# Optimization experiments

Measured on AMD Instinct MI355X. Metric: run time of the kernel, lower is better.

Reference implementation:

```python
import jax, jax.numpy as jnp
import numpy as np

IN_DIM = 18 * 2 * 1 * 536  # 19296
H = 512
OUT = 11
STEPS = 1024


def setup_inputs() -> dict:
    key = jax.random.key(0)
    ks = jax.random.split(key, 14)
    s = 0.02  # small init scale for stable LSTM dynamics
    f32 = jnp.float32
    return {
        "inputs": jax.random.normal(ks[0], (STEPS, IN_DIM), dtype=f32),
        "W_in": jax.random.normal(ks[1], (H, IN_DIM), dtype=f32) * s,
        "b_in": jnp.zeros((H,), dtype=f32),
        "Wih0": jax.random.normal(ks[2], (4 * H, H), dtype=f32) * s,
        "Whh0": jax.random.normal(ks[3], (4 * H, H), dtype=f32) * s,
        "bih0": jnp.zeros((4 * H,), dtype=f32),
        "bhh0": jnp.zeros((4 * H,), dtype=f32),
        "Wih1": jax.random.normal(ks[4], (4 * H, H), dtype=f32) * s,
        "Whh1": jax.random.normal(ks[5], (4 * H, H), dtype=f32) * s,
        "bih1": jnp.zeros((4 * H,), dtype=f32),
        "bhh1": jnp.zeros((4 * H,), dtype=f32),
        "W_out": jax.random.normal(ks[6], (OUT, H), dtype=f32) * s,
        "b_out": jnp.zeros((OUT,), dtype=f32),
    }


def _lstm_cell(gates, c):
    # PyTorch gate order: input, forget, cell(g), output
    i, f, g, o = jnp.split(gates, 4, axis=-1)
    c_new = jax.nn.sigmoid(f) * c + jax.nn.sigmoid(i) * jnp.tanh(g)
    h_new = jax.nn.sigmoid(o) * jnp.tanh(c_new)
    return h_new, c_new


def reference(inputs, W_in, b_in, Wih0, Whh0, bih0, bhh0,
              Wih1, Whh1, bih1, bhh1, W_out, b_out):
    # Input projection is time-independent -> batch it across all steps.
    x_proj = inputs @ W_in.T + b_in            # (STEPS, H)
    gx0 = x_proj @ Wih0.T + bih0               # (STEPS, 4H) precomputed layer-0 input gates

    def step(carry, gx0_t):
        h0, c0, h1, c1 = carry
        h0, c0 = _lstm_cell(gx0_t + h0 @ Whh0.T + bhh0, c0)
        h1, c1 = _lstm_cell(h0 @ Wih1.T + bih1 + h1 @ Whh1.T + bhh1, c1)
        return (h0, c0, h1, c1), h1

    z = jnp.zeros((H,), dtype=inputs.dtype)
    (h0, c0, h1, c1), hs = jax.lax.scan(step, (z, z, z, z), gx0)
    outputs = (hs @ W_out.T + b_out)[:, None, :]   # (STEPS, 1, OUT) == torch (steps, batch=1, 11)
    hn = jnp.stack([h0, h1])[:, None, :]           # (num_layers=2, batch=1, H)
    cn = jnp.stack([c0, c1])[:, None, :]
    return outputs, hn, cn
```

## Files before the change

### kernel.cpp

```cpp
#include <hip/hip_runtime.h>
#include <math.h>

typedef unsigned long long ull;
typedef unsigned int u32;
typedef unsigned short u16;
typedef _Float16 half2v __attribute__((ext_vector_type(2)));
typedef __bf16 bf16x8 __attribute__((ext_vector_type(8)));
typedef float f32x4 __attribute__((ext_vector_type(4)));

#define H 512
#define STEPS 1024
#define OUTN 11

__device__ __forceinline__ float sigm(float x) { return 1.f / (1.f + __expf(-x)); }
__device__ __forceinline__ ull ld_pair(const ull* p) {
  return __hip_atomic_load((ull*)p, __ATOMIC_RELAXED, __HIP_MEMORY_SCOPE_AGENT);
}
__device__ __forceinline__ void st_pair(ull* p, ull v) {
  __hip_atomic_store(p, v, __ATOMIC_RELAXED, __HIP_MEMORY_SCOPE_AGENT);
}
__device__ __forceinline__ float dot2acc(half2v a, half2v b, float c) {
#if __has_builtin(__builtin_amdgcn_fdot2)
  return __builtin_amdgcn_fdot2(a, b, c, false);
#else
  return c + (float)a.x * (float)b.x + (float)a.y * (float)b.y;
#endif
}
__device__ __forceinline__ u16 f16bits(float x) {
  return __builtin_bit_cast(u16, (_Float16)x);
}
__device__ __forceinline__ half2v bch2(u32 u) { return __builtin_bit_cast(half2v, u); }

__device__ __forceinline__ u32 split_bf16(float x) {
  u32 u = __float_as_uint(x);
  u32 rh = (u + 0x7FFFu + ((u >> 16) & 1u)) & 0xFFFF0000u;
  float hf = __uint_as_float(rh);
  float lo = x - hf;
  u32 ul = __float_as_uint(lo);
  u32 rl = (ul + 0x7FFFu + ((ul >> 16) & 1u)) & 0xFFFF0000u;
  return (rh >> 16) | rl;
}

__global__ void cvt_split(float* __restrict__ A, float* __restrict__ B, int nA, int n4) {
  int idx = blockIdx.x * 256 + threadIdx.x;
  if (idx >= n4) return;
  int base = idx * 4;
  float* p = (base < nA) ? (A + base) : (B + (base - nA));
  float4 v = *(float4*)p;
  u32 r0 = split_bf16(v.x), r1 = split_bf16(v.y), r2 = split_bf16(v.z), r3 = split_bf16(v.w);
  uint4 o = make_uint4(r0, r1, r2, r3);
  *(uint4*)p = o;
}

__global__ __launch_bounds__(256, 2)
void gemm_hilo(const u32* __restrict__ A2, const u32* __restrict__ B2,
               float* __restrict__ C, int M, int N, int K)
{
  __shared__ __align__(16) u16 Ah[64 * 32], Al[64 * 32], Bh[64 * 32], Bl[64 * 32];
  const int z = blockIdx.z;
  const int zstart = z * 151;
  const int nsteps = (z < 3) ? 151 : 150;
  const int mt = blockIdx.x * 64, nt = blockIdx.y * 64;
  const int tid = threadIdx.x;
  const int row = tid >> 2, cg = (tid & 3) * 8;
  const int wave = tid >> 6, lane = tid & 63;
  const int wm = (wave & 1) * 32, wn = (wave >> 1) * 32;
  const int quad = lane >> 4, l16 = lane & 15;

  f32x4 acc[2][2];
#pragma unroll
  for (int i = 0; i < 2; ++i)
#pragma unroll
    for (int j = 0; j < 2; ++j) acc[i][j] = (f32x4)0.f;

  for (int s = 0; s < nsteps; ++s) {
    const int kb = (zstart + s) * 32;
    {
      const u32* ap = A2 + (size_t)(mt + row) * K + kb + cg;
      const u32* bp = B2 + (size_t)(nt + row) * K + kb + cg;
      uint4 a0 = *(const uint4*)ap, a1 = *(const uint4*)(ap + 4);
      uint4 b0 = *(const uint4*)bp, b1 = *(const uint4*)(bp + 4);
      uint4 hi, lo;
      hi = make_uint4((a0.x & 0xFFFF) | (a0.y << 16), (a0.z & 0xFFFF) | (a0.w << 16),
                      (a1.x & 0xFFFF) | (a1.y << 16), (a1.z & 0xFFFF) | (a1.w << 16));
      lo = make_uint4((a0.x >> 16) | (a0.y & 0xFFFF0000u), (a0.z >> 16) | (a0.w & 0xFFFF0000u),
                      (a1.x >> 16) | (a1.y & 0xFFFF0000u), (a1.z >> 16) | (a1.w & 0xFFFF0000u));
      *(uint4*)&Ah[row * 32 + cg] = hi;
      *(uint4*)&Al[row * 32 + cg] = lo;
      hi = make_uint4((b0.x & 0xFFFF) | (b0.y << 16), (b0.z & 0xFFFF) | (b0.w << 16),
                      (b1.x & 0xFFFF) | (b1.y << 16), (b1.z & 0xFFFF) | (b1.w << 16));
      lo = make_uint4((b0.x >> 16) | (b0.y & 0xFFFF0000u), (b0.z >> 16) | (b0.w & 0xFFFF0000u),
                      (b1.x >> 16) | (b1.y & 0xFFFF0000u), (b1.z >> 16) | (b1.w & 0xFFFF0000u));
      *(uint4*)&Bh[row * 32 + cg] = hi;
      *(uint4*)&Bl[row * 32 + cg] = lo;
    }
    __syncthreads();
    bf16x8 ah[2], al[2], bh[2], bl[2];
#pragma unroll
    for (int mf = 0; mf < 2; ++mf) {
      int r = (wm + mf * 16 + l16) * 32 + quad * 8;
      ah[mf] = *reinterpret_cast<const bf16x8*>(&Ah[r]);
      al[mf] = *reinterpret_cast<const bf16x8*>(&Al[r]);
    }
#pragma unroll
    for (int nf = 0; nf < 2; ++nf) {
      int r = (wn + nf * 16 + l16) * 32 + quad * 8;
      bh[nf] = *reinterpret_cast<const bf16x8*>(&Bh[r]);
      bl[nf] = *reinterpret_cast<const bf16x8*>(&Bl[r]);
    }
#pragma unroll
    for (int mf = 0; mf < 2; ++mf)
#pragma unroll
      for (int nf = 0; nf < 2; ++nf) {
        acc[mf][nf] = __builtin_amdgcn_mfma_f32_16x16x32_bf16(ah[mf], bh[nf], acc[mf][nf], 0, 0, 0);
        acc[mf][nf] = __builtin_amdgcn_mfma_f32_16x16x32_bf16(ah[mf], bl[nf], acc[mf][nf], 0, 0, 0);
        acc[mf][nf] = __builtin_amdgcn_mfma_f32_16x16x32_bf16(al[mf], bh[nf], acc[mf][nf], 0, 0, 0);
      }
    __syncthreads();
  }

#pragma unroll
  for (int mf = 0; mf < 2; ++mf)
#pragma unroll
    for (int nf = 0; nf < 2; ++nf)
#pragma unroll
      for (int r = 0; r < 4; ++r) {
        int rw = mt + wm + mf * 16 + quad * 4 + r;
        int cl = nt + wn + nf * 16 + l16;
        atomicAdd(&C[(size_t)rw * N + cl], acc[mf][nf][r]);
      }
}

#define GBM 64
#define GBN 64
#define GBK 64
#define GLD 76

__global__ __launch_bounds__(256, 2)
void gemm_nt(const float* __restrict__ A, const float* __restrict__ B,
             float* __restrict__ C, const float* __restrict__ bias,
             int M, int N, int K)
{
  __shared__ float As[GBM][GLD];
  __shared__ float Bs[GBN][GLD];
  const int mt = blockIdx.x, nt = blockIdx.y;
  const int tid = threadIdx.x;
  const int tx = tid & 15, ty = tid >> 4;

  float acc[4][4] = {{0.f}};

  for (int kb = 0; kb < K; kb += GBK) {
#pragma unroll
    for (int i = 0; i < 4; ++i) {
      int r = ty + i * 16;
      int gk = kb + tx * 4;
      *(float4*)&As[r][tx * 4] = *(const float4*)(A + (size_t)(mt * GBM + r) * K + gk);
      *(float4*)&Bs[r][tx * 4] = *(const float4*)(B + (size_t)(nt * GBN + r) * K + gk);
    }
    __syncthreads();
#pragma unroll
    for (int k4 = 0; k4 < GBK; k4 += 4) {
      float4 a[4], b[4];
#pragma unroll
      for (int i = 0; i < 4; ++i) a[i] = *(const float4*)&As[ty * 4 + i][k4];
#pragma unroll
      for (int j = 0; j < 4; ++j) b[j] = *(const float4*)&Bs[tx * 4 + j][k4];
#pragma unroll
      for (int i = 0; i < 4; ++i)
#pragma unroll
        for (int j = 0; j < 4; ++j) {
          acc[i][j] = fmaf(a[i].x, b[j].x, acc[i][j]);
          acc[i][j] = fmaf(a[i].y, b[j].y, acc[i][j]);
          acc[i][j] = fmaf(a[i].z, b[j].z, acc[i][j]);
          acc[i][j] = fmaf(a[i].w, b[j].w, acc[i][j]);
        }
    }
    __syncthreads();
  }

#pragma unroll
  for (int i = 0; i < 4; ++i) {
    int m = mt * GBM + ty * 4 + i;
#pragma unroll
    for (int j = 0; j < 4; ++j) {
      int n = nt * GBN + tx * 4 + j;
      C[(size_t)m * N + n] = acc[i][j] + bias[n];
    }
  }
}

__global__ void init_xproj(float* __restrict__ xp, const float* __restrict__ b_in) {
  int i = blockIdx.x * 256 + threadIdx.x;
  xp[i] = b_in[i & (H - 1)];
}

__global__ void out_proj(const float* __restrict__ hs1, const float* __restrict__ Wout,
                         const float* __restrict__ bout, float* __restrict__ out) {
  int idx = blockIdx.x * 256 + threadIdx.x;
  if (idx >= STEPS * OUTN) return;
  int t = idx / OUTN, o = idx - t * OUTN;
  const float* h = hs1 + t * H;
  const float* wr = Wout + o * H;
  float acc = 0.f;
#pragma unroll 4
  for (int i = 0; i < H; i += 4) {
    float4 hv = *(const float4*)(h + i);
    float4 wv = *(const float4*)(wr + i);
    acc = fmaf(hv.x, wv.x, acc);
    acc = fmaf(hv.y, wv.y, acc);
    acc = fmaf(hv.z, wv.z, acc);
    acc = fmaf(hv.w, wv.w, acc);
  }
  out[idx] = acc + bout[o];
}

#define NC0 24
#define NC1 16
#define RD 8

__global__ __launch_bounds__(512, 1)
void lstm_chains(const float* __restrict__ gx0,
                 const float* __restrict__ Whh0, const float* __restrict__ bhh0,
                 const float* __restrict__ Wih1, const float* __restrict__ Whh1,
                 const float* __restrict__ bih1, const float* __restrict__ bhh1,
                 float* __restrict__ hs1, float* __restrict__ out,
                 ull* __restrict__ mb0, ull* __restrict__ mb1,
                 int* __restrict__ flags1)
{
  const int wg = blockIdx.x;
  const int tid = threadIdx.x;
  const bool role0 = (wg < 8);

  __shared__ __align__(16) u32 hl_u[512];
  __shared__ __align__(16) float gbuf[256];
  __shared__ __align__(16) float gxb[256];

  half2v wgt[8][16];
  float bias[8];
  int rg, ch;

  if (role0) {
    rg = tid >> 4; ch = tid & 15;
    int g = rg >> 3, lub = (rg & 7) * 8;
    int growb = (g << 9) + (wg << 6) + lub;
    const float* wb = Whh0 + (size_t)growb * H + ch * 32;
#pragma unroll
    for (int r = 0; r < 8; ++r) {
      const float* wr = wb + (size_t)r * H;
#pragma unroll
      for (int j4 = 0; j4 < 8; ++j4) {
        float4 f = *(const float4*)(wr + j4 * 4);
        wgt[r][2 * j4]     = half2v{(_Float16)f.x, (_Float16)f.y};
        wgt[r][2 * j4 + 1] = half2v{(_Float16)f.z, (_Float16)f.w};
      }
      bias[r] = bhh0[growb + r];
    }
  } else {
    rg = tid >> 5; ch = tid & 31;
    int g = rg >> 2, lub = (rg & 3) * 8;
    int growb = (g << 9) + ((wg - 8) << 5) + lub;
    const float* wb = (ch < 16) ? (Whh1 + (size_t)growb * H + ch * 32)
                                : (Wih1 + (size_t)growb * H + (ch - 16) * 32);
#pragma unroll
    for (int r = 0; r < 8; ++r) {
      const float* wr = wb + (size_t)r * H;
#pragma unroll
      for (int j4 = 0; j4 < 8; ++j4) {
        float4 f = *(const float4*)(wr + j4 * 4);
        wgt[r][2 * j4]     = half2v{(_Float16)f.x, (_Float16)f.y};
        wgt[r][2 * j4 + 1] = half2v{(_Float16)f.z, (_Float16)f.w};
      }
      bias[r] = bih1[growb + r] + bhh1[growb + r];
    }
  }

  float c_state = 0.f, h_last = 0.f;

  if (role0) {
    const int w = wg;
    for (int t = 0; t < STEPS; ++t) {
      if (tid >= 256) {
        int j = tid - 256;
        gxb[j] = gx0[t * 2048 + ((j >> 6) << 9) + (w << 6) + (j & 63)];
        if (j < 16 && (t & 3) == 0 && t > 0) {
          int need = t - 4, f;
          do {
            f = __hip_atomic_load(&flags1[j], __ATOMIC_RELAXED, __HIP_MEMORY_SCOPE_AGENT);
          } while (f < need);
        }
      } else {
        const ull* src = mb0 + ((((w << 3) | ((t + RD - 1) & (RD - 1)))) << 8) + tid;
        ull p;
        do { p = ld_pair(src); } while ((unsigned)(p >> 32) != (unsigned)t);
        hl_u[tid] = (u32)p;
      }
      __syncthreads();

      float accv[8];
#pragma unroll
      for (int r = 0; r < 8; ++r) accv[r] = 0.f;
      {
        const u32* hp = hl_u + (ch << 4);
        uint4 q0 = *(const uint4*)hp;
        uint4 q1 = *(const uint4*)(hp + 4);
        uint4 q2 = *(const uint4*)(hp + 8);
        uint4 q3 = *(const uint4*)(hp + 12);
        half2v h2[16] = {bch2(q0.x), bch2(q0.y), bch2(q0.z), bch2(q0.w),
                         bch2(q1.x), bch2(q1.y), bch2(q1.z), bch2(q1.w),
                         bch2(q2.x), bch2(q2.y), bch2(q2.z), bch2(q2.w),
                         bch2(q3.x), bch2(q3.y), bch2(q3.z), bch2(q3.w)};
#pragma unroll
        for (int j = 0; j < 16; ++j)
#pragma unroll
          for (int r = 0; r < 8; ++r)
            accv[r] = dot2acc(wgt[r][j], h2[j], accv[r]);
      }
#pragma unroll
      for (int o = 1; o < 16; o <<= 1)
#pragma unroll
        for (int r = 0; r < 8; ++r)
          accv[r] += __shfl_xor(accv[r], o);
      if (ch == 0) {
        float4 ga = *(const float4*)&gxb[rg * 8];
        float4 gb = *(const float4*)&gxb[rg * 8 + 4];
        float4 o0 = make_float4(accv[0] + bias[0] + ga.x, accv[1] + bias[1] + ga.y,
                                accv[2] + bias[2] + ga.z, accv[3] + bias[3] + ga.w);
        float4 o1 = make_float4(accv[4] + bias[4] + gb.x, accv[5] + bias[5] + gb.y,
                                accv[6] + bias[6] + gb.z, accv[7] + bias[7] + gb.w);
        *(float4*)&gbuf[rg * 8] = o0;
        *(float4*)&gbuf[rg * 8 + 4] = o1;
      }
      __syncthreads();

      if (tid < 64) {
        float gi = gbuf[tid], gf = gbuf[64 + tid], gg = gbuf[128 + tid], go = gbuf[192 + tid];
        c_state = sigm(gf) * c_state + sigm(gi) * tanhf(gg);
        float hv = sigm(go) * tanhf(c_state);
        float hnb = __shfl_down(hv, 1);
        if ((tid & 1) == 0) {
          u32 payl = (u32)f16bits(hv) | ((u32)f16bits(hnb) << 16);
          ull pay = ((ull)(unsigned)(t + 1) << 32) | (ull)payl;
          const int slot = t & (RD - 1);
          const int pidx = (w << 5) + (tid >> 1);
#pragma unroll
          for (int c = 0; c < NC0; ++c)
            st_pair(mb0 + (((c << 3) | slot) << 8) + pidx, pay);
        }
        h_last = hv;
      }
    }
  } else {
    const int v = wg - 8;
    for (int tau = 1; tau <= STEPS; ++tau) {
      const int t = tau - 1;
      if (tid < 256) {
        const ull* q1 = mb1 + ((((v << 3) | ((t + RD - 1) & (RD - 1)))) << 8) + tid;
        ull p;
        do { p = ld_pair(q1); } while ((unsigned)(p >> 32) != (unsigned)t);
        hl_u[tid] = (u32)p;
      } else {
        const ull* q0 = mb0 + (((((8 + v) << 3) | (t & (RD - 1)))) << 8) + (tid - 256);
        ull p;
        do { p = ld_pair(q0); } while ((unsigned)(p >> 32) != (unsigned)(t + 1));
        hl_u[tid] = (u32)p;
      }
      __syncthreads();

      float accv[8];
#pragma unroll
      for (int r = 0; r < 8; ++r) accv[r] = 0.f;
      {
        const u32* hp = hl_u + (ch << 4);
        uint4 q0 = *(const uint4*)hp;
        uint4 q1 = *(const uint4*)(hp + 4);
        uint4 q2 = *(const uint4*)(hp + 8);
        uint4 q3 = *(const uint4*)(hp + 12);
        half2v h2[16] = {bch2(q0.x), bch2(q0.y), bch2(q0.z), bch2(q0.w),
                         bch2(q1.x), bch2(q1.y), bch2(q1.z), bch2(q1.w),
                         bch2(q2.x), bch2(q2.y), bch2(q2.z), bch2(q2.w),
                         bch2(q3.x), bch2(q3.y), bch2(q3.z), bch2(q3.w)};
#pragma unroll
        for (int j = 0; j < 16; ++j)
#pragma unroll
          for (int r = 0; r < 8; ++r)
            accv[r] = dot2acc(wgt[r][j], h2[j], accv[r]);
      }
#pragma unroll
      for (int o = 1; o < 32; o <<= 1)
#pragma unroll
        for (int r = 0; r < 8; ++r)
          accv[r] += __shfl_xor(accv[r], o);
      if (ch == 0) {
        float4 o0 = make_float4(accv[0] + bias[0], accv[1] + bias[1],
                                accv[2] + bias[2], accv[3] + bias[3]);
        float4 o1 = make_float4(accv[4] + bias[4], accv[5] + bias[5],
                                accv[6] + bias[6], accv[7] + bias[7]);
        *(float4*)&gbuf[rg * 8] = o0;
        *(float4*)&gbuf[rg * 8 + 4] = o1;
      }
      __syncthreads();

      if (tid < 32) {
        int u = (v << 5) + tid;
        float gi = gbuf[tid], gf = gbuf[32 + tid], gg = gbuf[64 + tid], go = gbuf[96 + tid];
        c_state = sigm(gf) * c_state + sigm(gi) * tanhf(gg);
        float hv = sigm(go) * tanhf(c_state);
        float hnb = __shfl_down(hv, 1);
        if ((tid & 1) == 0) {
          u32 payl = (u32)f16bits(hv) | ((u32)f16bits(hnb) << 16);
          ull pay = ((ull)(unsigned)(t + 1) << 32) | (ull)payl;
          const int slot = t & (RD - 1);
          const int pidx = (v << 4) + (tid >> 1);
#pragma unroll
          for (int c = 0; c < NC1; ++c)
            st_pair(mb1 + (((c << 3) | slot) << 8) + pidx, pay);
        }
        h_last = hv;
        hs1[t * H + u] = hv;
      }
      if (tid == 0)
        __hip_atomic_store(&flags1[v], tau, __ATOMIC_RELAXED, __HIP_MEMORY_SCOPE_AGENT);
    }
  }

  if (role0) {
    if (tid < 64) {
      int u = (wg << 6) + tid;
      out[STEPS * OUTN + u] = h_last;
      out[STEPS * OUTN + 2 * H + u] = c_state;
    }
  } else {
    if (tid < 32) {
      int u = ((wg - 8) << 5) + tid;
      out[STEPS * OUTN + H + u] = h_last;
      out[STEPS * OUTN + 3 * H + u] = c_state;
    }
  }
}

extern "C" void kernel_launch(void* const* d_in, const int* in_sizes, int n_in,
                              void* d_out, int out_size, void* d_ws, size_t ws_size,
                              hipStream_t stream)
{
  (void)in_sizes; (void)n_in; (void)out_size; (void)ws_size;
  float* inputs = (float*)d_in[0];
  float* W_in   = (float*)d_in[1];
  const float* b_in   = (const float*)d_in[2];
  const float* Wih0   = (const float*)d_in[3];
  const float* Whh0   = (const float*)d_in[4];
  const float* bih0   = (const float*)d_in[5];
  const float* bhh0   = (const float*)d_in[6];
  const float* Wih1   = (const float*)d_in[7];
  const float* Whh1   = (const float*)d_in[8];
  const float* bih1   = (const float*)d_in[9];
  const float* bhh1   = (const float*)d_in[10];
  const float* W_out  = (const float*)d_in[11];
  const float* b_out  = (const float*)d_in[12];
  float* out = (float*)d_out;
  float* ws = (float*)d_ws;

  float* xp  = ws;
  float* gx0 = ws + 524288;
  float* hs1 = ws + 524288 + 2097152;
  char* syncb = (char*)(ws + 3145728);
  ull* mb0 = (ull*)syncb;
  ull* mb1 = (ull*)(syncb + 24 * 8 * 256 * 8);
  int* flags1 = (int*)(syncb + (24 + 16) * 8 * 256 * 8);

  hipMemsetAsync(syncb, 0, (24 + 16) * 8 * 256 * 8 + 64, stream);

  {
    const int nA = STEPS * 19296;
    const int n4 = (nA + H * 19296) / 4;
    cvt_split<<<n4 / 256, 256, 0, stream>>>(inputs, W_in, nA, n4);
  }
  init_xproj<<<2048, 256, 0, stream>>>(xp, b_in);
  {
    dim3 g(16, 8, 4);
    gemm_hilo<<<g, 256, 0, stream>>>((const u32*)inputs, (const u32*)W_in, xp,
                                     1024, 512, 19296);
  }
  {
    dim3 g(16, 32, 1);
    gemm_nt<<<g, 256, 0, stream>>>(xp, Wih0, gx0, bih0, 1024, 2048, 512);
  }
  lstm_chains<<<24, 512, 0, stream>>>(gx0, Whh0, bhh0, Wih1, Whh1, bih1, bhh1,
                                      hs1, out, mb0, mb1, flags1);
  out_proj<<<44, 256, 0, stream>>>(hs1, W_out, b_out, out);
}
```

Baseline: 3.257 ms.

## Replace per-consumer mailbox replication with shared dual-path polling buffers

The LSTM recurrence kernel now launches 192 blocks but keeps only every eighth, so the 24 active workgroups likely land on the same XCD. Each producer now writes one shared mailbox with a workgroup-scope store plus an agent-scope backup store, instead of fanning its payload out to 24 or 16 per-consumer copies. Consumers poll the fast copy with sc0 loads, which are meant to hit the shared L2, and fall back to an agent-scope load every 16 tries. The goal is lower per-step cross-workgroup communication latency, at the cost of relying on block-to-XCD placement and non-coherent fast-path visibility for progress.

```diff
diff --git a/kernel.cpp b/kernel.cpp
--- a/kernel.cpp
+++ b/kernel.cpp
@@ -11,13 +11,43 @@
 #define H 512
 #define STEPS 1024
 #define OUTN 11
+#define RD 8
+#define NROLE 24
 
 __device__ __forceinline__ float sigm(float x) { return 1.f / (1.f + __expf(-x)); }
-__device__ __forceinline__ ull ld_pair(const ull* p) {
+
+__device__ __forceinline__ ull ld_sc0(const ull* p) {
+  ull v;
+  asm volatile("global_load_dwordx2 %0, %1, off sc0\n\ts_waitcnt vmcnt(0)"
+               : "=v"(v) : "v"(p) : "memory");
+  return v;
+}
+__device__ __forceinline__ ull ld_slow(const ull* p) {
   return __hip_atomic_load((ull*)p, __ATOMIC_RELAXED, __HIP_MEMORY_SCOPE_AGENT);
 }
-__device__ __forceinline__ void st_pair(ull* p, ull v) {
-  __hip_atomic_store(p, v, __ATOMIC_RELAXED, __HIP_MEMORY_SCOPE_AGENT);
+__device__ __forceinline__ void st_dual(ull* fast, ull* slow, ull v) {
+  __hip_atomic_store(fast, v, __ATOMIC_RELAXED, __HIP_MEMORY_SCOPE_WORKGROUP);
+  __hip_atomic_store(slow, v, __ATOMIC_RELAXED, __HIP_MEMORY_SCOPE_AGENT);
+}
+__device__ __forceinline__ ull poll_tag(const ull* fast, const ull* slow, unsigned tag) {
+  for (;;) {
+#pragma unroll 1
+    for (int i = 0; i < 16; ++i) {
+      ull p = ld_sc0(fast);
+      if ((unsigned)(p >> 32) == tag) return p;
+    }
+    ull p = ld_slow(slow);
+    if ((unsigned)(p >> 32) == tag) return p;
+  }
+}
+__device__ __forceinline__ void poll_ge(const ull* fast, const ull* slow, unsigned need) {
+  for (;;) {
+#pragma unroll 1
+    for (int i = 0; i < 16; ++i) {
+      if ((unsigned)ld_sc0(fast) >= need) return;
+    }
+    if ((unsigned)ld_slow(slow) >= need) return;
+  }
 }
 __device__ __forceinline__ float dot2acc(half2v a, half2v b, float c) {
 #if __has_builtin(__builtin_amdgcn_fdot2)
@@ -214,21 +244,19 @@
   out[idx] = acc + bout[o];
 }
 
-#define NC0 24
-#define NC1 16
-#define RD 8
-
 __global__ __launch_bounds__(512, 1)
 void lstm_chains(const float* __restrict__ gx0,
                  const float* __restrict__ Whh0, const float* __restrict__ bhh0,
                  const float* __restrict__ Wih1, const float* __restrict__ Whh1,
                  const float* __restrict__ bih1, const float* __restrict__ bhh1,
                  float* __restrict__ hs1, float* __restrict__ out,
-                 ull* __restrict__ mb0, ull* __restrict__ mb1,
-                 int* __restrict__ flags1)
+                 ull* __restrict__ hb0f, ull* __restrict__ hb0s,
+                 ull* __restrict__ hb1f, ull* __restrict__ hb1s,
+                 ull* __restrict__ flf, ull* __restrict__ fls)
 {
-  const int wg = blockIdx.x;
   const int tid = threadIdx.x;
+  if (blockIdx.x & 7) return;
+  const int wg = blockIdx.x >> 3;
   const bool role0 = (wg < 8);
 
   __shared__ __align__(16) u32 hl_u[512];
@@ -282,16 +310,11 @@
       if (tid >= 256) {
         int j = tid - 256;
         gxb[j] = gx0[t * 2048 + ((j >> 6) << 9) + (w << 6) + (j & 63)];
-        if (j < 16 && (t & 3) == 0 && t > 0) {
-          int need = t - 4, f;
-          do {
-            f = __hip_atomic_load(&flags1[j], __ATOMIC_RELAXED, __HIP_MEMORY_SCOPE_AGENT);
-          } while (f < need);
-        }
+        if (j < 16 && (t & 3) == 0 && t > 0)
+          poll_ge(&flf[j], &fls[j], (unsigned)(t - 4));
       } else {
-        const ull* src = mb0 + ((((w << 3) | ((t + RD - 1) & (RD - 1)))) << 8) + tid;
-        ull p;
-        do { p = ld_pair(src); } while ((unsigned)(p >> 32) != (unsigned)t);
+        const int off = ((((unsigned)(t + RD - 1)) & (RD - 1)) << 8) + tid;
+        ull p = poll_tag(hb0f + off, hb0s + off, (unsigned)t);
         hl_u[tid] = (u32)p;
       }
       __syncthreads();
@@ -340,11 +363,8 @@
         if ((tid & 1) == 0) {
           u32 payl = (u32)f16bits(hv) | ((u32)f16bits(hnb) << 16);
           ull pay = ((ull)(unsigned)(t + 1) << 32) | (ull)payl;
-          const int slot = t & (RD - 1);
-          const int pidx = (w << 5) + (tid >> 1);
-#pragma unroll
-          for (int c = 0; c < NC0; ++c)
-            st_pair(mb0 + (((c << 3) | slot) << 8) + pidx, pay);
+          const int off = (((unsigned)t & (RD - 1)) << 8) + (w << 5) + (tid >> 1);
+          st_dual(hb0f + off, hb0s + off, pay);
         }
         h_last = hv;
       }
@@ -354,14 +374,12 @@
     for (int tau = 1; tau <= STEPS; ++tau) {
       const int t = tau - 1;
       if (tid < 256) {
-        const ull* q1 = mb1 + ((((v << 3) | ((t + RD - 1) & (RD - 1)))) << 8) + tid;
-        ull p;
-        do { p = ld_pair(q1); } while ((unsigned)(p >> 32) != (unsigned)t);
+        const int off = ((((unsigned)(t + RD - 1)) & (RD - 1)) << 8) + tid;
+        ull p = poll_tag(hb1f + off, hb1s + off, (unsigned)t);
         hl_u[tid] = (u32)p;
       } else {
-        const ull* q0 = mb0 + (((((8 + v) << 3) | (t & (RD - 1)))) << 8) + (tid - 256);
-        ull p;
-        do { p = ld_pair(q0); } while ((unsigned)(p >> 32) != (unsigned)(t + 1));
+        const int off = (((unsigned)t & (RD - 1)) << 8) + (tid - 256);
+        ull p = poll_tag(hb0f + off, hb0s + off, (unsigned)(t + 1));
         hl_u[tid] = (u32)p;
       }
       __syncthreads();
@@ -409,17 +427,14 @@
         if ((tid & 1) == 0) {
           u32 payl = (u32)f16bits(hv) | ((u32)f16bits(hnb) << 16);
           ull pay = ((ull)(unsigned)(t + 1) << 32) | (ull)payl;
-          const int slot = t & (RD - 1);
-          const int pidx = (v << 4) + (tid >> 1);
-#pragma unroll
-          for (int c = 0; c < NC1; ++c)
-            st_pair(mb1 + (((c << 3) | slot) << 8) + pidx, pay);
+          const int off = (((unsigned)t & (RD - 1)) << 8) + (v << 4) + (tid >> 1);
+          st_dual(hb1f + off, hb1s + off, pay);
         }
         h_last = hv;
         hs1[t * H + u] = hv;
       }
       if (tid == 0)
-        __hip_atomic_store(&flags1[v], tau, __ATOMIC_RELAXED, __HIP_MEMORY_SCOPE_AGENT);
+        st_dual(&flf[v], &fls[v], (ull)(unsigned)tau);
     }
   }
 
@@ -463,11 +478,14 @@
   float* gx0 = ws + 524288;
   float* hs1 = ws + 524288 + 2097152;
   char* syncb = (char*)(ws + 3145728);
-  ull* mb0 = (ull*)syncb;
-  ull* mb1 = (ull*)(syncb + 24 * 8 * 256 * 8);
-  int* flags1 = (int*)(syncb + (24 + 16) * 8 * 256 * 8);
-
-  hipMemsetAsync(syncb, 0, (24 + 16) * 8 * 256 * 8 + 64, stream);
+  ull* hb0f = (ull*)syncb;
+  ull* hb0s = (ull*)(syncb + 16384);
+  ull* hb1f = (ull*)(syncb + 32768);
+  ull* hb1s = (ull*)(syncb + 49152);
+  ull* flf  = (ull*)(syncb + 65536);
+  ull* fls  = (ull*)(syncb + 65536 + 128);
+
+  hipMemsetAsync(syncb, 0, 65536 + 256, stream);
 
   {
     const int nA = STEPS * 19296;
@@ -484,7 +502,7 @@
     dim3 g(16, 32, 1);
     gemm_nt<<<g, 256, 0, stream>>>(xp, Wih0, gx0, bih0, 1024, 2048, 512);
   }
-  lstm_chains<<<24, 512, 0, stream>>>(gx0, Whh0, bhh0, Wih1, Whh1, bih1, bhh1,
-                                      hs1, out, mb0, mb1, flags1);
+  lstm_chains<<<192, 512, 0, stream>>>(gx0, Whh0, bhh0, Wih1, Whh1, bih1, bhh1,
+                                       hs1, out, hb0f, hb0s, hb1f, hb1s, flf, fls);
   out_proj<<<44, 256, 0, stream>>>(hs1, W_out, b_out, out);
 }
```

Result: slower. 4.381 ms (+34.5%).
